# Kernel tuning notes

Measured on AMD Instinct MI355X. Metric: run time of the kernel, lower is better.

The kernel has to match this reference:

```python
import jax, jax.numpy as jnp
import numpy as np

N, E, B = 50000, 100000, 512   # nodes, edges, graphs
H, F_NODE, F_EDGE, T_OUT = 64, 16, 8, 1
T = 3                           # message-passing steps


def setup_inputs() -> dict:
    key = jax.random.key(0)
    ks = jax.random.split(key, 18)

    def w(k, shape, fan_in):
        return jax.random.normal(k, shape, dtype=jnp.float32) / np.sqrt(fan_in)

    return {
        "node_features": jax.random.normal(ks[0], (N, F_NODE), dtype=jnp.float32),
        "edge_features": jax.random.normal(ks[1], (E, F_EDGE), dtype=jnp.float32),
        "Esrc": jax.random.randint(ks[2], (E,), 0, N, dtype=jnp.int32),
        "Etgt": jax.random.randint(ks[3], (E,), 0, N, dtype=jnp.int32),
        "batch": jnp.sort(jax.random.randint(ks[4], (N,), 0, B, dtype=jnp.int32)),
        # input linear: node_features -> hidden
        "Win": w(ks[5], (H, F_NODE), F_NODE),
        "bin_": jnp.zeros((H,), jnp.float32),
        # edge encoder MLP: edge_features -> hidden -> hidden*hidden
        "We1": w(ks[6], (H, F_EDGE), F_EDGE),
        "be1": jnp.zeros((H,), jnp.float32),
        "We2": w(ks[7], (H * H, H), H),
        "be2": jnp.zeros((H * H,), jnp.float32),
        # GRU cell (shared across T steps)
        "Wih": w(ks[8], (3 * H, H), H),
        "bih": jnp.zeros((3 * H,), jnp.float32),
        "Whh": w(ks[9], (3 * H, H), H),
        "bhh": jnp.zeros((3 * H,), jnp.float32),
        # output linear: hidden -> target_features
        "Wout": w(ks[10], (T_OUT, H), H),
        "bout": jnp.zeros((T_OUT,), jnp.float32),
    }


def _gru(x, h, Wih, bih, Whh, bhh):
    gi = x @ Wih.T + bih            # [N, 3H]
    gh = h @ Whh.T + bhh
    i_r, i_z, i_n = jnp.split(gi, 3, axis=-1)
    h_r, h_z, h_n = jnp.split(gh, 3, axis=-1)
    r = jax.nn.sigmoid(i_r + h_r)
    z = jax.nn.sigmoid(i_z + h_z)
    n = jnp.tanh(i_n + r * h_n)
    return (1.0 - z) * n + z * h


def reference(node_features, edge_features, Esrc, Etgt, batch,
              Win, bin_, We1, be1, We2, be2,
              Wih, bih, Whh, bhh, Wout, bout):
    # Edge encoder MLP -> per-edge [H, H] message matrix (ENN style)
    eh = jax.nn.relu(edge_features @ We1.T + be1)          # [E, H]
    edge_data = (eh @ We2.T + be2).reshape(E, H, H)        # [E, H, H]

    x = node_features @ Win.T + bin_                       # [N, H]

    for _ in range(T):  # small fixed layer count
        msg = jnp.einsum('eij,ej->ei', edge_data, x[Esrc])  # per-edge matvec
        agg = jax.ops.segment_sum(msg, Etgt, num_segments=N)
        x = _gru(agg, x, Wih, bih, Whh, bhh)

    out = x @ Wout.T + bout                                # [N, 1]
    pooled = jax.ops.segment_sum(out, batch, num_segments=B)  # [B, 1]
    return pooled
```

## Files before the change

kernel.cpp:

```cpp
#include <hip/hip_runtime.h>
#include <hip/hip_fp16.h>

#define NN 50000
#define NE 100000
#define NB 512

typedef _Float16 f16x8 __attribute__((ext_vector_type(8)));
typedef _Float16 f16x4 __attribute__((ext_vector_type(4)));
typedef float f32x4  __attribute__((ext_vector_type(4)));
typedef float f32x16 __attribute__((ext_vector_type(16)));

__device__ __forceinline__ float sigm(float v) { return 1.0f / (1.0f + __expf(-v)); }
__device__ __forceinline__ float tanh_fast(float v) {
    float e = __expf(-2.0f * fabsf(v));
    float t = (1.0f - e) / (1.0f + e);
    return v < 0.f ? -t : t;
}

__global__ void fill0_kernel(float4* __restrict__ p, int n4)
{
    int i = blockIdx.x * 256 + threadIdx.x;
    const int stride = gridDim.x * 256;
    for (; i < n4; i += stride) p[i] = make_float4(0.f, 0.f, 0.f, 0.f);
}

__global__ __launch_bounds__(256) void node_in_kernel(
    const float* __restrict__ nf, const float* __restrict__ Win,
    const float* __restrict__ bin_, __half* __restrict__ xh)
{
    int idx = blockIdx.x * 256 + threadIdx.x;
    if (idx >= NN * 64) return;
    int n = idx >> 6, h = idx & 63;
    float acc = bin_[h];
    #pragma unroll
    for (int f = 0; f < 16; f++) acc += nf[n * 16 + f] * Win[h * 16 + f];
    xh[idx] = __float2half(acc);
}

__global__ __launch_bounds__(256) void edge_l1_kernel(
    const float* __restrict__ ef, const float* __restrict__ We1,
    const float* __restrict__ be1, __half* __restrict__ ehh)
{
    int idx = blockIdx.x * 256 + threadIdx.x;
    if (idx >= NE * 64) return;
    int e = idx >> 6, k = idx & 63;
    float acc = be1[k];
    #pragma unroll
    for (int f = 0; f < 8; f++) acc += ef[e * 8 + f] * We1[k * 8 + f];
    ehh[idx] = __float2half(fmaxf(acc, 0.0f));
}

__global__ __launch_bounds__(256) void pack_b32_kernel(
    const float* __restrict__ We2, const float* __restrict__ be2,
    __half* __restrict__ Bp)
{
    int idx = blockIdx.x * 256 + threadIdx.x;
    if (idx >= 260 * 1024) return;
    int i  = idx & 7;
    int n  = (idx >> 3) & 31;
    int hi = (idx >> 8) & 1;
    int nt = (idx >> 9) & 1;
    int kt = idx >> 10;
    int p  = kt * 16 + hi * 8 + i;
    int col = nt * 32 + n;
    float v;
    if (p < 4096) {
        int j = p >> 6, k = p & 63;
        v = We2[((size_t)(col * 64 + j)) * 64 + k];
    } else {
        v = be2[col * 64 + (p - 4096)];
    }
    Bp[idx] = __float2half(v);
}

__global__ __launch_bounds__(256) void pack_gru_kernel(
    const float* __restrict__ Wih, const float* __restrict__ Whh,
    __half* __restrict__ WG)
{
    int idx = blockIdx.x * 256 + threadIdx.x;
    if (idx >= 24576) return;
    int kk = idx & 31;
    int n  = (idx >> 5) & 15;
    int nt = (idx >> 9) % 24;
    int kt = (idx >> 9) / 24;
    int k = kt * 32 + kk;
    int col192 = (nt % 12) * 16 + n;
    int gate = col192 >> 6, h = col192 & 63;
    const float* src = (nt < 12) ? Wih : Whh;
    WG[idx] = __float2half(src[((size_t)(gate * 64 + h)) * 64 + k]);
}

__global__ __launch_bounds__(128, 2) void msg_kernel(
    const __half* __restrict__ xh, const __half* __restrict__ ehh,
    const __half* __restrict__ Bp,
    const int* __restrict__ Esrc, const int* __restrict__ Etgt,
    float* __restrict__ agg)
{
    __shared__ __attribute__((aligned(16))) __half xs[256 * 72];
    __shared__ int tgt_s[256];
    const int tid = threadIdx.x;
    const int eblk = blockIdx.x >> 1, ksel = blockIdx.x & 1;
    const int e0 = eblk * 256;
    const int w = tid >> 6, lane = tid & 63;
    const int n32 = lane & 31, hi = lane >> 5;

    #pragma unroll
    for (int rr = 0; rr < 2; rr++) {
        const int row = rr * 128 + tid;
        const int e = e0 + row;
        const bool ok = (e < NE);
        const int src = ok ? Esrc[e] : 0;
        tgt_s[row] = ok ? Etgt[e] : -1;
        const uint4* xsrc = (const uint4*)(xh + (size_t)src * 64);
        #pragma unroll
        for (int i = 0; i < 8; i++) {
            uint4 v = ok ? xsrc[i] : make_uint4(0, 0, 0, 0);
            *(uint4*)(&xs[row * 72 + i * 8]) = v;
        }
    }

    __half2 ehc[4][4][4];
    #pragma unroll
    for (int mt = 0; mt < 4; mt++) {
        const int e = e0 + w * 128 + mt * 32 + n32;
        if (e < NE) {
            #pragma unroll
            for (int c4 = 0; c4 < 4; c4++) {
                union { uint4 u; __half2 h[4]; } u;
                u.u = *(const uint4*)(ehh + (size_t)e * 64 + c4 * 16 + hi * 8);
                #pragma unroll
                for (int q = 0; q < 4; q++) ehc[mt][c4][q] = u.h[q];
            }
        } else {
            __half2 z = __half2half2(__float2half(0.f));
            #pragma unroll
            for (int c4 = 0; c4 < 4; c4++)
                #pragma unroll
                for (int q = 0; q < 4; q++) ehc[mt][c4][q] = z;
        }
    }
    __syncthreads();

    f32x16 acc[4][2];
    #pragma unroll
    for (int a = 0; a < 4; a++)
        #pragma unroll
        for (int b = 0; b < 2; b++)
            #pragma unroll
            for (int q = 0; q < 16; q++) acc[a][b][q] = 0.f;

    const int rbase = w * 128;
    const __half* bbase = Bp + (size_t)ksel * 131072 + hi * 256 + n32 * 8;

    #pragma unroll 1
    for (int g = 0; g < 8; g++) {
        const int jb = ksel * 32 + g * 4;
        f16x4 xr4[4];
        #pragma unroll
        for (int mt = 0; mt < 4; mt++)
            xr4[mt] = *(const f16x4*)(xs + (rbase + mt * 32 + n32) * 72 + jb);
        #pragma unroll
        for (int u = 0; u < 16; u++) {
            const __half* bp = bbase + (size_t)(g * 16 + u) * 1024;
            f16x8 b0 = *(const f16x8*)(bp);
            f16x8 b1 = *(const f16x8*)(bp + 512);
            const int c4 = u & 3;
            const int jq = u >> 2;
            #pragma unroll
            for (int mt = 0; mt < 4; mt++) {
                union { f16x4 v; __half h[4]; } xu; xu.v = xr4[mt];
                __half2 xv2 = __half2half2(xu.h[jq]);
                union { __half2 h[4]; f16x8 v; } a;
                #pragma unroll
                for (int q = 0; q < 4; q++) a.h[q] = __hmul2(xv2, ehc[mt][c4][q]);
                acc[mt][0] = __builtin_amdgcn_mfma_f32_32x32x16_f16(a.v, b0, acc[mt][0], 0, 0, 0);
                acc[mt][1] = __builtin_amdgcn_mfma_f32_32x32x16_f16(a.v, b1, acc[mt][1], 0, 0, 0);
            }
        }
    }

    if (ksel) {
        #pragma unroll
        for (int u = 0; u < 4; u++) {
            const __half* bp = Bp + (size_t)(256 + u) * 1024 + hi * 256 + n32 * 8;
            f16x8 b0 = *(const f16x8*)(bp);
            f16x8 b1 = *(const f16x8*)(bp + 512);
            #pragma unroll
            for (int mt = 0; mt < 4; mt++) {
                f16x8 a = *(const f16x8*)(xs + (rbase + mt * 32 + n32) * 72 + u * 16 + hi * 8);
                acc[mt][0] = __builtin_amdgcn_mfma_f32_32x32x16_f16(a, b0, acc[mt][0], 0, 0, 0);
                acc[mt][1] = __builtin_amdgcn_mfma_f32_32x32x16_f16(a, b1, acc[mt][1], 0, 0, 0);
            }
        }
    }

    #pragma unroll
    for (int mt = 0; mt < 4; mt++) {
        #pragma unroll
        for (int r = 0; r < 16; r++) {
            const int rowe = (r & 3) + 8 * (r >> 2) + 4 * hi;
            const int t = tgt_s[rbase + mt * 32 + rowe];
            if (t >= 0) {
                atomicAdd(agg + (size_t)t * 64 + n32, acc[mt][0][r]);
                atomicAdd(agg + (size_t)t * 64 + 32 + n32, acc[mt][1][r]);
            }
        }
    }
}

__global__ __launch_bounds__(256, 2) void gru_kernel(
    float* __restrict__ agg, __half* __restrict__ xh,
    const __half* __restrict__ WG,
    const float* __restrict__ bih, const float* __restrict__ bhh)
{
    __shared__ __attribute__((aligned(16))) __half wlds[24576];
    __shared__ __attribute__((aligned(16))) __half aggh[64 * 72];
    __shared__ __attribute__((aligned(16))) __half xhs[64 * 72];
    const int tid = threadIdx.x;
    const int node0 = blockIdx.x * 64;

    {
        const uint4* src = (const uint4*)WG;
        uint4* dst = (uint4*)wlds;
        #pragma unroll
        for (int i = 0; i < 12; i++) dst[i * 256 + tid] = src[i * 256 + tid];
    }
    #pragma unroll
    for (int i = 0; i < 4; i++) {
        int idx4 = i * 256 + tid;
        int nl = idx4 >> 4, c4 = idx4 & 15;
        int node = node0 + nl;
        float4 a = make_float4(0.f, 0.f, 0.f, 0.f);
        if (node < NN) a = *(const float4*)(agg + (size_t)node * 64 + c4 * 4);
        __half2* ah = (__half2*)(aggh + nl * 72 + c4 * 4);
        ah[0] = __floats2half2_rn(a.x, a.y);
        ah[1] = __floats2half2_rn(a.z, a.w);
    }
    #pragma unroll
    for (int i = 0; i < 2; i++) {
        int idx8 = i * 256 + tid;
        int nl = idx8 >> 3, c8 = idx8 & 7;
        int node = node0 + nl;
        uint4 v = make_uint4(0, 0, 0, 0);
        if (node < NN) v = *(const uint4*)(xh + (size_t)node * 64 + c8 * 8);
        *(uint4*)(&xhs[nl * 72 + c8 * 8]) = v;
    }
    __syncthreads();

    const int w = tid >> 6, lane = tid & 63, m = lane & 15, quad = lane >> 4;
    const int nl_a = w * 16 + m;

    f16x8 a_agg[2], a_x[2];
    #pragma unroll
    for (int kt = 0; kt < 2; kt++) {
        const int koff = kt * 32 + quad * 8;
        a_agg[kt] = *(const f16x8*)(aggh + nl_a * 72 + koff);
        a_x[kt]   = *(const f16x8*)(xhs  + nl_a * 72 + koff);
    }

    f32x4 acc[24];
    #pragma unroll
    for (int nt = 0; nt < 24; nt++)
        #pragma unroll
        for (int q = 0; q < 4; q++) acc[nt][q] = 0.f;

    #pragma unroll
    for (int kt = 0; kt < 2; kt++) {
        #pragma unroll
        for (int nt = 0; nt < 24; nt++) {
            f16x8 b = *(const f16x8*)(wlds + (kt * 24 + nt) * 512 + m * 32 + quad * 8);
            acc[nt] = __builtin_amdgcn_mfma_f32_16x16x32_f16(
                (nt < 12) ? a_agg[kt] : a_x[kt], b, acc[nt], 0, 0, 0);
        }
    }

    #pragma unroll
    for (int t = 0; t < 4; t++) {
        const int h = t * 16 + m;
        const float bir = bih[h], biz = bih[64 + h], bin = bih[128 + h];
        const float bhr = bhh[h], bhz = bhh[64 + h], bhn = bhh[128 + h];
        #pragma unroll
        for (int r = 0; r < 4; r++) {
            const int nl = w * 16 + quad * 4 + r;
            float ir  = acc[t][r]      + bir;
            float iz  = acc[4 + t][r]  + biz;
            float in_ = acc[8 + t][r]  + bin;
            float hr  = acc[12 + t][r] + bhr;
            float hz  = acc[16 + t][r] + bhz;
            float hn  = acc[20 + t][r] + bhn;
            float rg = sigm(ir + hr);
            float z  = sigm(iz + hz);
            float n  = tanh_fast(in_ + rg * hn);
            float xold = __half2float(xhs[nl * 72 + h]);
            xhs[nl * 72 + h] = __float2half((1.0f - z) * n + z * xold);
        }
    }
    __syncthreads();

    #pragma unroll
    for (int i = 0; i < 2; i++) {
        int idx8 = i * 256 + tid;
        int nl = idx8 >> 3, c8 = idx8 & 7;
        int node = node0 + nl;
        if (node < NN)
            *(uint4*)(xh + (size_t)node * 64 + c8 * 8) = *(const uint4*)(&xhs[nl * 72 + c8 * 8]);
    }
    #pragma unroll
    for (int i = 0; i < 4; i++) {
        int idx4 = i * 256 + tid;
        int nl = idx4 >> 4, c4 = idx4 & 15;
        int node = node0 + nl;
        if (node < NN)
            *(float4*)(agg + (size_t)node * 64 + c4 * 4) = make_float4(0.f, 0.f, 0.f, 0.f);
    }
}

__global__ __launch_bounds__(256, 2) void gru_pool_kernel(
    const float* __restrict__ agg, const __half* __restrict__ xh,
    const __half* __restrict__ WG,
    const float* __restrict__ bih, const float* __restrict__ bhh,
    const float* __restrict__ Wout, const float* __restrict__ bout,
    const int* __restrict__ batch, float* __restrict__ out)
{
    __shared__ __attribute__((aligned(16))) __half wlds[24576];
    __shared__ __attribute__((aligned(16))) __half aggh[64 * 72];
    __shared__ __attribute__((aligned(16))) __half xhs[64 * 72];
    const int tid = threadIdx.x;
    const int node0 = blockIdx.x * 64;

    {
        const uint4* src = (const uint4*)WG;
        uint4* dst = (uint4*)wlds;
        #pragma unroll
        for (int i = 0; i < 12; i++) dst[i * 256 + tid] = src[i * 256 + tid];
    }
    #pragma unroll
    for (int i = 0; i < 4; i++) {
        int idx4 = i * 256 + tid;
        int nl = idx4 >> 4, c4 = idx4 & 15;
        int node = node0 + nl;
        float4 a = make_float4(0.f, 0.f, 0.f, 0.f);
        if (node < NN) a = *(const float4*)(agg + (size_t)node * 64 + c4 * 4);
        __half2* ah = (__half2*)(aggh + nl * 72 + c4 * 4);
        ah[0] = __floats2half2_rn(a.x, a.y);
        ah[1] = __floats2half2_rn(a.z, a.w);
    }
    #pragma unroll
    for (int i = 0; i < 2; i++) {
        int idx8 = i * 256 + tid;
        int nl = idx8 >> 3, c8 = idx8 & 7;
        int node = node0 + nl;
        uint4 v = make_uint4(0, 0, 0, 0);
        if (node < NN) v = *(const uint4*)(xh + (size_t)node * 64 + c8 * 8);
        *(uint4*)(&xhs[nl * 72 + c8 * 8]) = v;
    }
    __syncthreads();

    const int w = tid >> 6, lane = tid & 63, m = lane & 15, quad = lane >> 4;
    const int nl_a = w * 16 + m;
    const int nbase = node0 + w * 16;

    f16x8 a_agg[2], a_x[2];
    #pragma unroll
    for (int kt = 0; kt < 2; kt++) {
        const int koff = kt * 32 + quad * 8;
        a_agg[kt] = *(const f16x8*)(aggh + nl_a * 72 + koff);
        a_x[kt]   = *(const f16x8*)(xhs  + nl_a * 72 + koff);
    }

    f32x4 acc[24];
    #pragma unroll
    for (int nt = 0; nt < 24; nt++)
        #pragma unroll
        for (int q = 0; q < 4; q++) acc[nt][q] = 0.f;

    #pragma unroll
    for (int kt = 0; kt < 2; kt++) {
        #pragma unroll
        for (int nt = 0; nt < 24; nt++) {
            f16x8 b = *(const f16x8*)(wlds + (kt * 24 + nt) * 512 + m * 32 + quad * 8);
            acc[nt] = __builtin_amdgcn_mfma_f32_16x16x32_f16(
                (nt < 12) ? a_agg[kt] : a_x[kt], b, acc[nt], 0, 0, 0);
        }
    }

    float po[4] = {0.f, 0.f, 0.f, 0.f};
    #pragma unroll
    for (int t = 0; t < 4; t++) {
        const int h = t * 16 + m;
        const float bir = bih[h], biz = bih[64 + h], bin = bih[128 + h];
        const float bhr = bhh[h], bhz = bhh[64 + h], bhn = bhh[128 + h];
        const float wo = Wout[h];
        #pragma unroll
        for (int r = 0; r < 4; r++) {
            const int nl = w * 16 + quad * 4 + r;
            float ir  = acc[t][r]      + bir;
            float iz  = acc[4 + t][r]  + biz;
            float in_ = acc[8 + t][r]  + bin;
            float hr  = acc[12 + t][r] + bhr;
            float hz  = acc[16 + t][r] + bhz;
            float hn  = acc[20 + t][r] + bhn;
            float rg = sigm(ir + hr);
            float z  = sigm(iz + hz);
            float n  = tanh_fast(in_ + rg * hn);
            float xold = __half2float(xhs[nl * 72 + h]);
            float xn = (1.0f - z) * n + z * xold;
            po[r] += xn * wo;
        }
    }
    #pragma unroll
    for (int off = 1; off < 16; off <<= 1) {
        #pragma unroll
        for (int r = 0; r < 4; r++) po[r] += __shfl_xor(po[r], off, 64);
    }
    if (m == 0) {
        const float b0 = bout[0];
        #pragma unroll
        for (int r = 0; r < 4; r++) {
            const int nd = nbase + quad * 4 + r;
            if (nd < NN) atomicAdd(out + batch[nd], po[r] + b0);
        }
    }
}

extern "C" void kernel_launch(void* const* d_in, const int* in_sizes, int n_in,
                              void* d_out, int out_size, void* d_ws, size_t ws_size,
                              hipStream_t stream)
{
    const float* nf   = (const float*)d_in[0];
    const float* ef   = (const float*)d_in[1];
    const int*   Esrc = (const int*)  d_in[2];
    const int*   Etgt = (const int*)  d_in[3];
    const int*   bat  = (const int*)  d_in[4];
    const float* Win  = (const float*)d_in[5];
    const float* bin_ = (const float*)d_in[6];
    const float* We1  = (const float*)d_in[7];
    const float* be1  = (const float*)d_in[8];
    const float* We2  = (const float*)d_in[9];
    const float* be2  = (const float*)d_in[10];
    const float* Wih  = (const float*)d_in[11];
    const float* bih  = (const float*)d_in[12];
    const float* Whh  = (const float*)d_in[13];
    const float* bhh  = (const float*)d_in[14];
    const float* Wout = (const float*)d_in[15];
    const float* bout = (const float*)d_in[16];

    char* ws = (char*)d_ws;
    float*  agg = (float*)(ws);
    __half* xh  = (__half*)(ws + 12800000);
    __half* ehh = (__half*)(ws + 19200000);
    __half* Bp  = (__half*)(ws + 32000000);
    __half* WG  = (__half*)(ws + 32600064);

    hipMemsetAsync(d_out, 0, NB * sizeof(float), stream);

    fill0_kernel<<<1024, 256, 0, stream>>>((float4*)agg, NN * 16);
    node_in_kernel<<<(NN * 64 + 255) / 256, 256, 0, stream>>>(nf, Win, bin_, xh);
    edge_l1_kernel<<<(NE * 64 + 255) / 256, 256, 0, stream>>>(ef, We1, be1, ehh);
    pack_b32_kernel<<<(260 * 1024 + 255) / 256, 256, 0, stream>>>(We2, be2, Bp);
    pack_gru_kernel<<<(24576 + 255) / 256, 256, 0, stream>>>(Wih, Whh, WG);

    const int msg_grid = 2 * ((NE + 255) / 256);
    for (int t = 0; t < 2; t++) {
        msg_kernel<<<msg_grid, 128, 0, stream>>>(xh, ehh, Bp, Esrc, Etgt, agg);
        gru_kernel<<<(NN + 63) / 64, 256, 0, stream>>>(agg, xh, WG, bih, bhh);
    }
    msg_kernel<<<msg_grid, 128, 0, stream>>>(xh, ehh, Bp, Esrc, Etgt, agg);
    gru_pool_kernel<<<(NN + 63) / 64, 256, 0, stream>>>(
        agg, xh, WG, bih, bhh, Wout, bout, bat, (float*)d_out);
}
```

Before: 522.4 us.

## Stage edge-weight tiles in LDS with double buffering; fuse prologue kernels

The message kernel now gives each block 128 edges and the full K range, removing the old two-way K split across blocks. Each step streams a 16 KB tile of the packed We2 matrix through a double-buffered shared-memory stage, so the block shares one copy instead of every wave reading global memory directly. This halves the number of atomic adds to agg, since partial sums are no longer split across two blocks. The five setup kernels and the memset are merged into one block-range dispatched prologue kernel to cut launch overhead, at the cost of more LDS per block and a barrier every step.

```diff
diff --git a/kernel.cpp b/kernel.cpp
--- a/kernel.cpp
+++ b/kernel.cpp
@@ -17,77 +17,72 @@
     return v < 0.f ? -t : t;
 }
 
-__global__ void fill0_kernel(float4* __restrict__ p, int n4)
+#define S0 12500
+#define S1 (S0 + 25000)
+#define S2 (S1 + 1056)
+#define S3 (S2 + 96)
+#define S4 (S3 + 3125)
+#define S5 (S4 + 2)
+__global__ __launch_bounds__(256) void prologue_kernel(
+    const float* __restrict__ nf, const float* __restrict__ Win, const float* __restrict__ bin_,
+    const float* __restrict__ ef, const float* __restrict__ We1, const float* __restrict__ be1,
+    const float* __restrict__ We2, const float* __restrict__ be2,
+    const float* __restrict__ Wih, const float* __restrict__ Whh,
+    __half* __restrict__ xh, __half* __restrict__ ehh,
+    __half* __restrict__ Bp, __half* __restrict__ WG,
+    float* __restrict__ agg, float* __restrict__ outp)
 {
-    int i = blockIdx.x * 256 + threadIdx.x;
-    const int stride = gridDim.x * 256;
-    for (; i < n4; i += stride) p[i] = make_float4(0.f, 0.f, 0.f, 0.f);
-}
-
-__global__ __launch_bounds__(256) void node_in_kernel(
-    const float* __restrict__ nf, const float* __restrict__ Win,
-    const float* __restrict__ bin_, __half* __restrict__ xh)
-{
-    int idx = blockIdx.x * 256 + threadIdx.x;
-    if (idx >= NN * 64) return;
-    int n = idx >> 6, h = idx & 63;
-    float acc = bin_[h];
-    #pragma unroll
-    for (int f = 0; f < 16; f++) acc += nf[n * 16 + f] * Win[h * 16 + f];
-    xh[idx] = __float2half(acc);
-}
-
-__global__ __launch_bounds__(256) void edge_l1_kernel(
-    const float* __restrict__ ef, const float* __restrict__ We1,
-    const float* __restrict__ be1, __half* __restrict__ ehh)
-{
-    int idx = blockIdx.x * 256 + threadIdx.x;
-    if (idx >= NE * 64) return;
-    int e = idx >> 6, k = idx & 63;
-    float acc = be1[k];
-    #pragma unroll
-    for (int f = 0; f < 8; f++) acc += ef[e * 8 + f] * We1[k * 8 + f];
-    ehh[idx] = __float2half(fmaxf(acc, 0.0f));
-}
-
-__global__ __launch_bounds__(256) void pack_b32_kernel(
-    const float* __restrict__ We2, const float* __restrict__ be2,
-    __half* __restrict__ Bp)
-{
-    int idx = blockIdx.x * 256 + threadIdx.x;
-    if (idx >= 260 * 1024) return;
-    int i  = idx & 7;
-    int n  = (idx >> 3) & 31;
-    int hi = (idx >> 8) & 1;
-    int nt = (idx >> 9) & 1;
-    int kt = idx >> 10;
-    int p  = kt * 16 + hi * 8 + i;
-    int col = nt * 32 + n;
-    float v;
-    if (p < 4096) {
-        int j = p >> 6, k = p & 63;
-        v = We2[((size_t)(col * 64 + j)) * 64 + k];
+    const int b = blockIdx.x;
+    if (b < S0) {
+        int idx = b * 256 + threadIdx.x;
+        int n = idx >> 6, h = idx & 63;
+        float acc = bin_[h];
+        #pragma unroll
+        for (int f = 0; f < 16; f++) acc += nf[n * 16 + f] * Win[h * 16 + f];
+        xh[idx] = __float2half(acc);
+    } else if (b < S1) {
+        int idx = (b - S0) * 256 + threadIdx.x;
+        int e = idx >> 6, k = idx & 63;
+        float acc = be1[k];
+        #pragma unroll
+        for (int f = 0; f < 8; f++) acc += ef[e * 8 + f] * We1[k * 8 + f];
+        ehh[idx] = __float2half(fmaxf(acc, 0.0f));
+    } else if (b < S2) {
+        int idx = (b - S1) * 256 + threadIdx.x;
+        int i  = idx & 7;
+        int n  = (idx >> 3) & 31;
+        int hi = (idx >> 8) & 1;
+        int nt = (idx >> 9) & 1;
+        int kt = idx >> 10;
+        int p  = kt * 16 + hi * 8 + i;
+        int col = nt * 32 + n;
+        float v = 0.f;
+        if (p < 4096) {
+            int j = p >> 6, k = p & 63;
+            v = We2[((size_t)(col * 64 + j)) * 64 + k];
+        } else if (p < 4160) {
+            v = be2[col * 64 + (p - 4096)];
+        }
+        Bp[idx] = __float2half(v);
+    } else if (b < S3) {
+        int idx = (b - S2) * 256 + threadIdx.x;
+        int kk = idx & 31;
+        int n  = (idx >> 5) & 15;
+        int nt = (idx >> 9) % 24;
+        int kt = (idx >> 9) / 24;
+        int k = kt * 32 + kk;
+        int col192 = (nt % 12) * 16 + n;
+        int gate = col192 >> 6, h = col192 & 63;
+        const float* src = (nt < 12) ? Wih : Whh;
+        WG[idx] = __float2half(src[((size_t)(gate * 64 + h)) * 64 + k]);
+    } else if (b < S4) {
+        int idx = (b - S3) * 256 + threadIdx.x;
+        if (idx < NN * 16)
+            *((float4*)agg + idx) = make_float4(0.f, 0.f, 0.f, 0.f);
     } else {
-        v = be2[col * 64 + (p - 4096)];
-    }
-    Bp[idx] = __float2half(v);
-}
-
-__global__ __launch_bounds__(256) void pack_gru_kernel(
-    const float* __restrict__ Wih, const float* __restrict__ Whh,
-    __half* __restrict__ WG)
-{
-    int idx = blockIdx.x * 256 + threadIdx.x;
-    if (idx >= 24576) return;
-    int kk = idx & 31;
-    int n  = (idx >> 5) & 15;
-    int nt = (idx >> 9) % 24;
-    int kt = (idx >> 9) / 24;
-    int k = kt * 32 + kk;
-    int col192 = (nt % 12) * 16 + n;
-    int gate = col192 >> 6, h = col192 & 63;
-    const float* src = (nt < 12) ? Wih : Whh;
-    WG[idx] = __float2half(src[((size_t)(gate * 64 + h)) * 64 + k]);
+        int idx = (b - S4) * 256 + threadIdx.x;
+        if (idx < NB) outp[idx] = 0.f;
+    }
 }
 
 __global__ __launch_bounds__(128, 2) void msg_kernel(
@@ -96,33 +91,31 @@
     const int* __restrict__ Esrc, const int* __restrict__ Etgt,
     float* __restrict__ agg)
 {
-    __shared__ __attribute__((aligned(16))) __half xs[256 * 72];
-    __shared__ int tgt_s[256];
+    __shared__ __attribute__((aligned(16))) __half xs[128 * 72];
+    __shared__ __attribute__((aligned(16))) __half bst[2][8192];
+    __shared__ int tgt_s[128];
     const int tid = threadIdx.x;
-    const int eblk = blockIdx.x >> 1, ksel = blockIdx.x & 1;
-    const int e0 = eblk * 256;
+    const int e0 = blockIdx.x * 128;
     const int w = tid >> 6, lane = tid & 63;
     const int n32 = lane & 31, hi = lane >> 5;
 
-    #pragma unroll
-    for (int rr = 0; rr < 2; rr++) {
-        const int row = rr * 128 + tid;
-        const int e = e0 + row;
+    {
+        const int e = e0 + tid;
         const bool ok = (e < NE);
         const int src = ok ? Esrc[e] : 0;
-        tgt_s[row] = ok ? Etgt[e] : -1;
+        tgt_s[tid] = ok ? Etgt[e] : -1;
         const uint4* xsrc = (const uint4*)(xh + (size_t)src * 64);
         #pragma unroll
         for (int i = 0; i < 8; i++) {
             uint4 v = ok ? xsrc[i] : make_uint4(0, 0, 0, 0);
-            *(uint4*)(&xs[row * 72 + i * 8]) = v;
-        }
-    }
-
-    __half2 ehc[4][4][4];
-    #pragma unroll
-    for (int mt = 0; mt < 4; mt++) {
-        const int e = e0 + w * 128 + mt * 32 + n32;
+            *(uint4*)(&xs[tid * 72 + i * 8]) = v;
+        }
+    }
+
+    __half2 ehc[2][4][4];
+    #pragma unroll
+    for (int mt = 0; mt < 2; mt++) {
+        const int e = e0 + w * 64 + mt * 32 + n32;
         if (e < NE) {
             #pragma unroll
             for (int c4 = 0; c4 < 4; c4++) {
@@ -139,63 +132,82 @@
                 for (int q = 0; q < 4; q++) ehc[mt][c4][q] = z;
         }
     }
+
+    f32x16 acc[2][2];
+    #pragma unroll
+    for (int a = 0; a < 2; a++)
+        #pragma unroll
+        for (int b = 0; b < 2; b++)
+            #pragma unroll
+            for (int q = 0; q < 16; q++) acc[a][b][q] = 0.f;
+
+    const int rbase = w * 64;
+    const uint4* gB = (const uint4*)Bp;
+
+    uint4 breg[8];
+    #pragma unroll
+    for (int i = 0; i < 8; i++) breg[i] = gB[i * 128 + tid];
+    #pragma unroll
+    for (int i = 0; i < 8; i++) *(uint4*)(&bst[0][(i * 128 + tid) * 8]) = breg[i];
     __syncthreads();
 
-    f32x16 acc[4][2];
-    #pragma unroll
-    for (int a = 0; a < 4; a++)
-        #pragma unroll
-        for (int b = 0; b < 2; b++)
-            #pragma unroll
-            for (int q = 0; q < 16; q++) acc[a][b][q] = 0.f;
-
-    const int rbase = w * 128;
-    const __half* bbase = Bp + (size_t)ksel * 131072 + hi * 256 + n32 * 8;
-
     #pragma unroll 1
-    for (int g = 0; g < 8; g++) {
-        const int jb = ksel * 32 + g * 4;
-        f16x4 xr4[4];
-        #pragma unroll
-        for (int mt = 0; mt < 4; mt++)
-            xr4[mt] = *(const f16x4*)(xs + (rbase + mt * 32 + n32) * 72 + jb);
-        #pragma unroll
-        for (int u = 0; u < 16; u++) {
-            const __half* bp = bbase + (size_t)(g * 16 + u) * 1024;
-            f16x8 b0 = *(const f16x8*)(bp);
-            f16x8 b1 = *(const f16x8*)(bp + 512);
-            const int c4 = u & 3;
-            const int jq = u >> 2;
-            #pragma unroll
-            for (int mt = 0; mt < 4; mt++) {
-                union { f16x4 v; __half h[4]; } xu; xu.v = xr4[mt];
-                __half2 xv2 = __half2half2(xu.h[jq]);
-                union { __half2 h[4]; f16x8 v; } a;
+    for (int c = 0; c < 33; c++) {
+        const int buf = c & 1;
+        if (c + 1 < 33) {
+            #pragma unroll
+            for (int i = 0; i < 8; i++) breg[i] = gB[(c + 1) * 1024 + i * 128 + tid];
+        }
+        const __half* blane = bst[buf] + hi * 256 + n32 * 8;
+
+        if (c < 32) {
+            __half xj[2][2];
+            #pragma unroll
+            for (int mt = 0; mt < 2; mt++) {
+                __half2 t = *(const __half2*)(xs + (rbase + mt * 32 + n32) * 72 + c * 2);
+                xj[mt][0] = t.x; xj[mt][1] = t.y;
+            }
+            #pragma unroll
+            for (int u = 0; u < 8; u++) {
+                f16x8 b0 = *(const f16x8*)(blane + u * 1024);
+                f16x8 b1 = *(const f16x8*)(blane + u * 1024 + 512);
+                const int c4 = u & 3;
+                const int jq = u >> 2;
                 #pragma unroll
-                for (int q = 0; q < 4; q++) a.h[q] = __hmul2(xv2, ehc[mt][c4][q]);
-                acc[mt][0] = __builtin_amdgcn_mfma_f32_32x32x16_f16(a.v, b0, acc[mt][0], 0, 0, 0);
-                acc[mt][1] = __builtin_amdgcn_mfma_f32_32x32x16_f16(a.v, b1, acc[mt][1], 0, 0, 0);
+                for (int mt = 0; mt < 2; mt++) {
+                    __half2 xv2 = __half2half2(xj[mt][jq]);
+                    union { __half2 h[4]; f16x8 v; } a;
+                    #pragma unroll
+                    for (int q = 0; q < 4; q++) a.h[q] = __hmul2(xv2, ehc[mt][c4][q]);
+                    acc[mt][0] = __builtin_amdgcn_mfma_f32_32x32x16_f16(a.v, b0, acc[mt][0], 0, 0, 0);
+                    acc[mt][1] = __builtin_amdgcn_mfma_f32_32x32x16_f16(a.v, b1, acc[mt][1], 0, 0, 0);
+                }
             }
-        }
-    }
-
-    if (ksel) {
-        #pragma unroll
-        for (int u = 0; u < 4; u++) {
-            const __half* bp = Bp + (size_t)(256 + u) * 1024 + hi * 256 + n32 * 8;
-            f16x8 b0 = *(const f16x8*)(bp);
-            f16x8 b1 = *(const f16x8*)(bp + 512);
-            #pragma unroll
-            for (int mt = 0; mt < 4; mt++) {
-                f16x8 a = *(const f16x8*)(xs + (rbase + mt * 32 + n32) * 72 + u * 16 + hi * 8);
-                acc[mt][0] = __builtin_amdgcn_mfma_f32_32x32x16_f16(a, b0, acc[mt][0], 0, 0, 0);
-                acc[mt][1] = __builtin_amdgcn_mfma_f32_32x32x16_f16(a, b1, acc[mt][1], 0, 0, 0);
+        } else {
+            #pragma unroll
+            for (int u = 0; u < 8; u++) {
+                f16x8 b0 = *(const f16x8*)(blane + u * 1024);
+                f16x8 b1 = *(const f16x8*)(blane + u * 1024 + 512);
+                const int v = u & 3;
+                #pragma unroll
+                for (int mt = 0; mt < 2; mt++) {
+                    f16x8 a = *(const f16x8*)(xs + (rbase + mt * 32 + n32) * 72 + v * 16 + hi * 8);
+                    acc[mt][0] = __builtin_amdgcn_mfma_f32_32x32x16_f16(a, b0, acc[mt][0], 0, 0, 0);
+                    acc[mt][1] = __builtin_amdgcn_mfma_f32_32x32x16_f16(a, b1, acc[mt][1], 0, 0, 0);
+                }
             }
         }
-    }
-
-    #pragma unroll
-    for (int mt = 0; mt < 4; mt++) {
+
+        if (c + 1 < 33) {
+            #pragma unroll
+            for (int i = 0; i < 8; i++)
+                *(uint4*)(&bst[buf ^ 1][(i * 128 + tid) * 8]) = breg[i];
+        }
+        __syncthreads();
+    }
+
+    #pragma unroll
+    for (int mt = 0; mt < 2; mt++) {
         #pragma unroll
         for (int r = 0; r < 16; r++) {
             const int rowe = (r & 3) + 8 * (r >> 2) + 4 * hi;
@@ -452,15 +464,11 @@
     __half* Bp  = (__half*)(ws + 32000000);
     __half* WG  = (__half*)(ws + 32600064);
 
-    hipMemsetAsync(d_out, 0, NB * sizeof(float), stream);
-
-    fill0_kernel<<<1024, 256, 0, stream>>>((float4*)agg, NN * 16);
-    node_in_kernel<<<(NN * 64 + 255) / 256, 256, 0, stream>>>(nf, Win, bin_, xh);
-    edge_l1_kernel<<<(NE * 64 + 255) / 256, 256, 0, stream>>>(ef, We1, be1, ehh);
-    pack_b32_kernel<<<(260 * 1024 + 255) / 256, 256, 0, stream>>>(We2, be2, Bp);
-    pack_gru_kernel<<<(24576 + 255) / 256, 256, 0, stream>>>(Wih, Whh, WG);
-
-    const int msg_grid = 2 * ((NE + 255) / 256);
+    prologue_kernel<<<S5, 256, 0, stream>>>(
+        nf, Win, bin_, ef, We1, be1, We2, be2, Wih, Whh,
+        xh, ehh, Bp, WG, agg, (float*)d_out);
+
+    const int msg_grid = (NE + 127) / 128;
     for (int t = 0; t < 2; t++) {
         msg_kernel<<<msg_grid, 128, 0, stream>>>(xh, ehh, Bp, Esrc, Etgt, agg);
         gru_kernel<<<(NN + 63) / 64, 256, 0, stream>>>(agg, xh, WG, bih, bhh);
```

Measured after the change: 734.3 us. 1.41x slower.
